# Kernel optimization log

Hardware: AMD Instinct MI355X
Metric: run time of the kernel (lower is better)

The kernel has to match this reference:

```python
import jax, jax.numpy as jnp
import numpy as np

K = 255
L = 1.0 / K
W = L / 2.5
MU = (L * (jnp.arange(K, dtype=jnp.float32) + 0.5))  # [K]


def soft_hist(x):
    # x: [B, H, W] -> [B, K] soft histogram (mean of sigmoid-window memberships)
    B = x.shape[0]
    N = x.shape[1] * x.shape[2]
    xf = x.reshape(B, 1, -1)                      # [B, 1, N]
    d = xf - MU[None, :, None]                    # [B, K, N]
    pj = jax.nn.sigmoid((d + L / 2) / W) - jax.nn.sigmoid((d - L / 2) / W)
    return pj.sum(axis=2) / N                     # [B, K]


def emd(x, y):
    # matmul with lower-triangular ones == cumulative sum along bins
    cdf_x = jnp.cumsum(x, axis=1)
    cdf_y = jnp.cumsum(y, axis=1)
    return jnp.sum(jnp.square(cdf_x - cdf_y), axis=1)  # [B]


def setup_inputs() -> dict:
    key = jax.random.key(0)
    k1, k2 = jax.random.split(key)
    img = jax.random.uniform(k1, (8, 3, 256, 256), dtype=jnp.float32)
    img_t = jax.random.uniform(k2, (8, 3, 256, 256), dtype=jnp.float32)
    return {"img": img, "img_t": img_t}


def reference(img, img_t):
    r, g, b = img[:, 0], img[:, 1], img[:, 2]
    r_t, g_t, b_t = img_t[:, 0], img_t[:, 1], img_t[:, 2]
    r_hist = soft_hist(r)
    g_hist = soft_hist(g)
    b_hist = soft_hist(b)
    r_t_hist = soft_hist(r_t)  # computed but unused, faithful to original (bug: earth(r_hist, r_hist))
    g_t_hist = soft_hist(g_t)
    b_t_hist = soft_hist(b_t)
    loss = emd(r_hist, r_hist) + emd(g_hist, g_t_hist) + emd(b_hist, b_t_hist)
    return loss  # [B]
```

## Files before the change

### kernel.cpp

```cpp
#include <hip/hip_runtime.h>


#define NT 256
#define QF 32
#define FB 8160
#define FBP 8192
#define PAD 96
#define CNT_LDS 8448

__device__ __forceinline__ float fsigmoid(float z) {
    return __builtin_amdgcn_rcpf(1.0f + __expf(-z));
}

__global__ __launch_bounds__(NT) void fine_hist_kernel(
    const float* __restrict__ img, const float* __restrict__ img_t,
    unsigned* __restrict__ ws, int sub, int pix)
{
    const int blk = blockIdx.x;
    const int h   = blk / sub;
    const int s   = blk - h * sub;
    const int b   = h >> 2;
    const int ch  = 1 + ((h >> 1) & 1);
    const float* src = (h & 1) ? img_t : img;
    const float4* base = (const float4*)(src + (size_t)(b * 3 + ch) * 65536u
                                             + (size_t)s * (size_t)pix);

    __shared__ unsigned hist[FBP];
    #pragma unroll
    for (int r = 0; r < 8; ++r)
        ((uint4*)hist)[threadIdx.x + NT * r] = make_uint4(0u, 0u, 0u, 0u);
    __syncthreads();

    const int nv = pix >> 2;
    for (int i = threadIdx.x; i < nv; i += NT) {
        const float4 v = base[i];
        int j0 = (int)(v.x * 8160.0f);
        int j1 = (int)(v.y * 8160.0f);
        int j2 = (int)(v.z * 8160.0f);
        int j3 = (int)(v.w * 8160.0f);
        j0 = j0 < 0 ? 0 : (j0 > FB - 1 ? FB - 1 : j0);
        j1 = j1 < 0 ? 0 : (j1 > FB - 1 ? FB - 1 : j1);
        j2 = j2 < 0 ? 0 : (j2 > FB - 1 ? FB - 1 : j2);
        j3 = j3 < 0 ? 0 : (j3 > FB - 1 ? FB - 1 : j3);
        atomicAdd(&hist[j0], 1u);
        atomicAdd(&hist[j1], 1u);
        atomicAdd(&hist[j2], 1u);
        atomicAdd(&hist[j3], 1u);
    }
    __syncthreads();

    uint4* o = (uint4*)(ws + (size_t)blk * (size_t)FBP);
    #pragma unroll
    for (int r = 0; r < 8; ++r)
        o[threadIdx.x + NT * r] = ((uint4*)hist)[threadIdx.x + NT * r];
}

__global__ __launch_bounds__(NT) void cdf_kernel(
    const unsigned* __restrict__ ws, float* __restrict__ cdfout, int sub)
{
    const int h = blockIdx.x;
    const int k = threadIdx.x;

    __shared__ float cnt[CNT_LDS];
    __shared__ float coarse[NT];
    __shared__ float red[4];

    float4 acc[8];
    #pragma unroll
    for (int r = 0; r < 8; ++r) acc[r] = make_float4(0.f, 0.f, 0.f, 0.f);
    for (int s = 0; s < sub; ++s) {
        const uint4* p = (const uint4*)(ws + (size_t)(h * sub + s) * (size_t)FBP);
        #pragma unroll
        for (int r = 0; r < 8; ++r) {
            const uint4 u = p[k + NT * r];
            acc[r].x += (float)u.x; acc[r].y += (float)u.y;
            acc[r].z += (float)u.z; acc[r].w += (float)u.w;
        }
    }
    #pragma unroll
    for (int r = 0; r < 8; ++r)
        ((float4*)(cnt + PAD))[k + NT * r] = acc[r];
    if (k < PAD) cnt[k] = 0.0f;
    if (k < CNT_LDS - PAD - FBP) cnt[PAD + FBP + k] = 0.0f;
    __syncthreads();

    float cc = 0.0f;
    #pragma unroll
    for (int q = 0; q < QF; ++q) {
        const int qq = (q + k) & (QF - 1);
        cc += cnt[PAD + QF * k + qq];
    }
    coarse[k] = cc;
    __syncthreads();

    for (int off = 1; off < NT; off <<= 1) {
        const float v = (k + off < NT) ? coarse[k + off] : 0.0f;
        __syncthreads();
        coarse[k] += v;
        __syncthreads();
    }

    float s0t = cnt[PAD + k] * fsigmoid(2.5f * ((float)k + 0.5f) / 32.0f);
    #pragma unroll
    for (int off = 32; off; off >>= 1) s0t += __shfl_down(s0t, off);
    if ((k & 63) == 0) red[k >> 6] = s0t;
    __syncthreads();
    const float S0 = red[0] + red[1] + red[2] + red[3] + coarse[8];

    float t = 0.0f;
    const int jbase = PAD + QF * (k - 3);
    for (int i = 0; i < 256; ++i) {
        const int m = (i + k) & 255;
        const float sg = fsigmoid(2.5f * ((float)m + 0.5f) * (1.0f / 32.0f) - 10.0f);
        t += cnt[jbase + m] * sg;
    }
    const float ones = (k + 5 < NT) ? coarse[k + 5] : 0.0f;

    float cdf = 0.0f;
    if (k <= 254) cdf = (S0 - (t + ones)) * (1.0f / 65536.0f);
    cdfout[h * NT + k] = cdf;
}

__global__ __launch_bounds__(NT) void emd_kernel(
    const float* __restrict__ cdf, float* __restrict__ out)
{
    const int b = blockIdx.x;
    const int k = threadIdx.x;
    const float* c0 = cdf + (size_t)(b * 4 + 0) * NT;
    const float* c1 = cdf + (size_t)(b * 4 + 1) * NT;
    const float* c2 = cdf + (size_t)(b * 4 + 2) * NT;
    const float* c3 = cdf + (size_t)(b * 4 + 3) * NT;

    float v = 0.0f;
    if (k <= 254) {
        const float dg = c0[k] - c1[k];
        const float db = c2[k] - c3[k];
        v = dg * dg + db * db;
    }
    #pragma unroll
    for (int off = 32; off; off >>= 1) v += __shfl_down(v, off);
    __shared__ float red[4];
    if ((k & 63) == 0) red[k >> 6] = v;
    __syncthreads();
    if (k == 0) out[b] = red[0] + red[1] + red[2] + red[3];
}

extern "C" void kernel_launch(void* const* d_in, const int* in_sizes, int n_in,
                              void* d_out, int out_size, void* d_ws, size_t ws_size,
                              hipStream_t stream)
{
    const float* img   = (const float*)d_in[0];
    const float* img_t = (const float*)d_in[1];
    float* out = (float*)d_out;

    int SUB = 8;
    while (SUB > 1 &&
           (size_t)(32 * SUB) * FBP * 4u + 32u * NT * 4u > ws_size) SUB >>= 1;
    const int pix = 65536 / SUB;

    unsigned* ws_hist = (unsigned*)d_ws;
    float*    ws_cdf  = (float*)d_ws + (size_t)(32 * SUB) * FBP;

    hipLaunchKernelGGL(fine_hist_kernel, dim3(32 * SUB), dim3(NT), 0, stream,
                       img, img_t, ws_hist, SUB, pix);
    hipLaunchKernelGGL(cdf_kernel, dim3(32), dim3(NT), 0, stream,
                       ws_hist, ws_cdf, SUB);
    hipLaunchKernelGGL(emd_kernel, dim3(8), dim3(NT), 0, stream,
                       ws_cdf, out);
}
```

Before: 82.06 us.

## Halve fine-bin resolution, add parallel merge kernel, fuse CDF with EMD

The fine histogram drops from 8160 to 4080 bins (16 per coarse bin), which halves the LDS footprint and the partial-histogram traffic. Sub-splitting rises to 16 blocks per histogram. A new 256-block merge kernel sums the partials in parallel, replacing the 32-block serial accumulation inside the CDF kernel. CDF and EMD are fused into one 1024-thread block per batch item that uses a precomputed sigmoid table. The coarser fine bins approximate the sigmoid convolution less closely, which may affect accuracy.

```diff
diff --git a/kernel.cpp b/kernel.cpp
--- a/kernel.cpp
+++ b/kernel.cpp
@@ -1,47 +1,49 @@
 #include <hip/hip_runtime.h>
 
 
-#define NT 256
-#define QF 32
-#define FB 8160
-#define FBP 8192
-#define PAD 96
-#define CNT_LDS 8448
+#define QF 16
+#define FBINS 4096
+#define FBV 4080
+#define PADL 64
+#define CNTSZ (PADL + FBINS + 64)
 
 __device__ __forceinline__ float fsigmoid(float z) {
     return __builtin_amdgcn_rcpf(1.0f + __expf(-z));
 }
 
-__global__ __launch_bounds__(NT) void fine_hist_kernel(
+template<int SUB>
+__global__ __launch_bounds__(256) void fine_hist_kernel(
     const float* __restrict__ img, const float* __restrict__ img_t,
-    unsigned* __restrict__ ws, int sub, int pix)
+    unsigned* __restrict__ part)
 {
     const int blk = blockIdx.x;
-    const int h   = blk / sub;
-    const int s   = blk - h * sub;
+    const int h   = blk / SUB;
+    const int s   = blk - h * SUB;
     const int b   = h >> 2;
     const int ch  = 1 + ((h >> 1) & 1);
     const float* src = (h & 1) ? img_t : img;
+    const int pix = 65536 / SUB;
     const float4* base = (const float4*)(src + (size_t)(b * 3 + ch) * 65536u
                                              + (size_t)s * (size_t)pix);
 
-    __shared__ unsigned hist[FBP];
+    __shared__ unsigned hist[FBINS];
+    uint4* h4 = (uint4*)hist;
     #pragma unroll
-    for (int r = 0; r < 8; ++r)
-        ((uint4*)hist)[threadIdx.x + NT * r] = make_uint4(0u, 0u, 0u, 0u);
+    for (int r = 0; r < 4; ++r)
+        h4[threadIdx.x + 256 * r] = make_uint4(0u, 0u, 0u, 0u);
     __syncthreads();
 
     const int nv = pix >> 2;
-    for (int i = threadIdx.x; i < nv; i += NT) {
+    for (int i = threadIdx.x; i < nv; i += 256) {
         const float4 v = base[i];
-        int j0 = (int)(v.x * 8160.0f);
-        int j1 = (int)(v.y * 8160.0f);
-        int j2 = (int)(v.z * 8160.0f);
-        int j3 = (int)(v.w * 8160.0f);
-        j0 = j0 < 0 ? 0 : (j0 > FB - 1 ? FB - 1 : j0);
-        j1 = j1 < 0 ? 0 : (j1 > FB - 1 ? FB - 1 : j1);
-        j2 = j2 < 0 ? 0 : (j2 > FB - 1 ? FB - 1 : j2);
-        j3 = j3 < 0 ? 0 : (j3 > FB - 1 ? FB - 1 : j3);
+        int j0 = (int)(v.x * 4080.0f);
+        int j1 = (int)(v.y * 4080.0f);
+        int j2 = (int)(v.z * 4080.0f);
+        int j3 = (int)(v.w * 4080.0f);
+        j0 = j0 < 0 ? 0 : (j0 > FBV - 1 ? FBV - 1 : j0);
+        j1 = j1 < 0 ? 0 : (j1 > FBV - 1 ? FBV - 1 : j1);
+        j2 = j2 < 0 ? 0 : (j2 > FBV - 1 ? FBV - 1 : j2);
+        j3 = j3 < 0 ? 0 : (j3 > FBV - 1 ? FBV - 1 : j3);
         atomicAdd(&hist[j0], 1u);
         atomicAdd(&hist[j1], 1u);
         atomicAdd(&hist[j2], 1u);
@@ -49,100 +51,119 @@
     }
     __syncthreads();
 
-    uint4* o = (uint4*)(ws + (size_t)blk * (size_t)FBP);
+    uint4* o = (uint4*)(part + (size_t)blk * (size_t)FBINS);
     #pragma unroll
-    for (int r = 0; r < 8; ++r)
-        o[threadIdx.x + NT * r] = ((uint4*)hist)[threadIdx.x + NT * r];
+    for (int r = 0; r < 4; ++r)
+        o[threadIdx.x + 256 * r] = h4[threadIdx.x + 256 * r];
 }
 
-__global__ __launch_bounds__(NT) void cdf_kernel(
-    const unsigned* __restrict__ ws, float* __restrict__ cdfout, int sub)
+template<int SUB>
+__global__ __launch_bounds__(256) void merge_kernel(
+    const unsigned* __restrict__ part, unsigned* __restrict__ merged)
 {
-    const int h = blockIdx.x;
-    const int k = threadIdx.x;
+    const int h = blockIdx.x >> 3;
+    const int c = blockIdx.x & 7;
+    const int t = threadIdx.x;
+    const unsigned* p0 = part + (size_t)h * SUB * FBINS + c * 512 + 2 * t;
+    unsigned ax = 0u, ay = 0u;
+    #pragma unroll
+    for (int s = 0; s < SUB; ++s) {
+        const uint2 u = *(const uint2*)(p0 + (size_t)s * FBINS);
+        ax += u.x; ay += u.y;
+    }
+    *(uint2*)(merged + (size_t)h * FBINS + c * 512 + 2 * t) = make_uint2(ax, ay);
+}
 
-    __shared__ float cnt[CNT_LDS];
-    __shared__ float coarse[NT];
-    __shared__ float red[4];
+__global__ __launch_bounds__(1024) void cdf_emd_kernel(
+    const unsigned* __restrict__ merged, float* __restrict__ out)
+{
+    const int b   = blockIdx.x;
+    const int tid = threadIdx.x;
+    const int sg  = tid >> 8;
+    const int k   = tid & 255;
 
-    float4 acc[8];
+    __shared__ float cnt[4][CNTSZ];
+    __shared__ float coarse[4][256];
+    __shared__ float sgt[128];
+    __shared__ float s0red[16];
+    __shared__ float cdfs[4][256];
+    __shared__ float lred[16];
+
+    if (tid < 128)
+        sgt[tid] = fsigmoid((2.5f / 16.0f) * ((float)tid + 0.5f) - 10.0f);
+
+    const uint4* src = (const uint4*)(merged + (size_t)(b * 4 + sg) * FBINS);
+    float* cn = cnt[sg];
     #pragma unroll
-    for (int r = 0; r < 8; ++r) acc[r] = make_float4(0.f, 0.f, 0.f, 0.f);
-    for (int s = 0; s < sub; ++s) {
-        const uint4* p = (const uint4*)(ws + (size_t)(h * sub + s) * (size_t)FBP);
-        #pragma unroll
-        for (int r = 0; r < 8; ++r) {
-            const uint4 u = p[k + NT * r];
-            acc[r].x += (float)u.x; acc[r].y += (float)u.y;
-            acc[r].z += (float)u.z; acc[r].w += (float)u.w;
-        }
+    for (int r = 0; r < 4; ++r) {
+        const uint4 u = src[k + 256 * r];
+        *(float4*)(cn + PADL + 4 * (k + 256 * r)) =
+            make_float4((float)u.x, (float)u.y, (float)u.z, (float)u.w);
     }
-    #pragma unroll
-    for (int r = 0; r < 8; ++r)
-        ((float4*)(cnt + PAD))[k + NT * r] = acc[r];
-    if (k < PAD) cnt[k] = 0.0f;
-    if (k < CNT_LDS - PAD - FBP) cnt[PAD + FBP + k] = 0.0f;
+    if (k < PADL) cn[k] = 0.0f;
+    if (k < CNTSZ - PADL - FBINS) cn[PADL + FBINS + k] = 0.0f;
     __syncthreads();
 
     float cc = 0.0f;
     #pragma unroll
     for (int q = 0; q < QF; ++q) {
         const int qq = (q + k) & (QF - 1);
-        cc += cnt[PAD + QF * k + qq];
+        cc += cn[PADL + QF * k + qq];
     }
-    coarse[k] = cc;
+    coarse[sg][k] = cc;
+
+    float s0p = 0.0f;
+    if (k < 64) s0p = cn[PADL + k] * fsigmoid((2.5f / 16.0f) * ((float)k + 0.5f));
+    #pragma unroll
+    for (int off = 32; off; off >>= 1) s0p += __shfl_down(s0p, off);
+    if ((tid & 63) == 0) s0red[tid >> 6] = s0p;
+    __syncthreads();
+    const float S0w = s0red[4 * sg] + s0red[4 * sg + 1]
+                    + s0red[4 * sg + 2] + s0red[4 * sg + 3];
+
+    for (int off = 1; off < 256; off <<= 1) {
+        const float v = (k + off < 256) ? coarse[sg][k + off] : 0.0f;
+        __syncthreads();
+        coarse[sg][k] += v;
+        __syncthreads();
+    }
+    const float S0 = S0w + coarse[sg][4];
+
+    float t = 0.0f;
+    const int jb = PADL + QF * k - 48;
+    for (int i = 0; i < 128; ++i) {
+        const int m = (i + k) & 127;
+        t += cn[jb + m] * sgt[m];
+    }
+    const float ones = (k + 5 < 256) ? coarse[sg][k + 5] : 0.0f;
+
+    cdfs[sg][k] = (k <= 254) ? (S0 - t - ones) * (1.0f / 65536.0f) : 0.0f;
     __syncthreads();
 
-    for (int off = 1; off < NT; off <<= 1) {
-        const float v = (k + off < NT) ? coarse[k + off] : 0.0f;
-        __syncthreads();
-        coarse[k] += v;
-        __syncthreads();
+    if (tid < 256) {
+        const float dg = cdfs[0][tid] - cdfs[1][tid];
+        const float db = cdfs[2][tid] - cdfs[3][tid];
+        float v = dg * dg + db * db;
+        #pragma unroll
+        for (int off = 32; off; off >>= 1) v += __shfl_down(v, off);
+        if ((tid & 63) == 0) lred[tid >> 6] = v;
     }
-
-    float s0t = cnt[PAD + k] * fsigmoid(2.5f * ((float)k + 0.5f) / 32.0f);
-    #pragma unroll
-    for (int off = 32; off; off >>= 1) s0t += __shfl_down(s0t, off);
-    if ((k & 63) == 0) red[k >> 6] = s0t;
     __syncthreads();
-    const float S0 = red[0] + red[1] + red[2] + red[3] + coarse[8];
-
-    float t = 0.0f;
-    const int jbase = PAD + QF * (k - 3);
-    for (int i = 0; i < 256; ++i) {
-        const int m = (i + k) & 255;
-        const float sg = fsigmoid(2.5f * ((float)m + 0.5f) * (1.0f / 32.0f) - 10.0f);
-        t += cnt[jbase + m] * sg;
-    }
-    const float ones = (k + 5 < NT) ? coarse[k + 5] : 0.0f;
-
-    float cdf = 0.0f;
-    if (k <= 254) cdf = (S0 - (t + ones)) * (1.0f / 65536.0f);
-    cdfout[h * NT + k] = cdf;
+    if (tid == 0) out[b] = lred[0] + lred[1] + lred[2] + lred[3];
 }
 
-__global__ __launch_bounds__(NT) void emd_kernel(
-    const float* __restrict__ cdf, float* __restrict__ out)
+template<int SUB>
+static void launch_all(const float* img, const float* img_t, float* out,
+                       void* d_ws, hipStream_t stream)
 {
-    const int b = blockIdx.x;
-    const int k = threadIdx.x;
-    const float* c0 = cdf + (size_t)(b * 4 + 0) * NT;
-    const float* c1 = cdf + (size_t)(b * 4 + 1) * NT;
-    const float* c2 = cdf + (size_t)(b * 4 + 2) * NT;
-    const float* c3 = cdf + (size_t)(b * 4 + 3) * NT;
-
-    float v = 0.0f;
-    if (k <= 254) {
-        const float dg = c0[k] - c1[k];
-        const float db = c2[k] - c3[k];
-        v = dg * dg + db * db;
-    }
-    #pragma unroll
-    for (int off = 32; off; off >>= 1) v += __shfl_down(v, off);
-    __shared__ float red[4];
-    if ((k & 63) == 0) red[k >> 6] = v;
-    __syncthreads();
-    if (k == 0) out[b] = red[0] + red[1] + red[2] + red[3];
+    unsigned* part   = (unsigned*)d_ws;
+    unsigned* merged = part + (size_t)32 * SUB * FBINS;
+    hipLaunchKernelGGL(fine_hist_kernel<SUB>, dim3(32 * SUB), dim3(256), 0, stream,
+                       img, img_t, part);
+    hipLaunchKernelGGL(merge_kernel<SUB>, dim3(256), dim3(256), 0, stream,
+                       part, merged);
+    hipLaunchKernelGGL(cdf_emd_kernel, dim3(8), dim3(1024), 0, stream,
+                       merged, out);
 }
 
 extern "C" void kernel_launch(void* const* d_in, const int* in_sizes, int n_in,
@@ -153,18 +174,10 @@
     const float* img_t = (const float*)d_in[1];
     float* out = (float*)d_out;
 
-    int SUB = 8;
-    while (SUB > 1 &&
-           (size_t)(32 * SUB) * FBP * 4u + 32u * NT * 4u > ws_size) SUB >>= 1;
-    const int pix = 65536 / SUB;
+    const size_t need16 = ((size_t)32 * 16 + 32) * FBINS * 4u;
+    const size_t need4  = ((size_t)32 * 4  + 32) * FBINS * 4u;
 
-    unsigned* ws_hist = (unsigned*)d_ws;
-    float*    ws_cdf  = (float*)d_ws + (size_t)(32 * SUB) * FBP;
-
-    hipLaunchKernelGGL(fine_hist_kernel, dim3(32 * SUB), dim3(NT), 0, stream,
-                       img, img_t, ws_hist, SUB, pix);
-    hipLaunchKernelGGL(cdf_kernel, dim3(32), dim3(NT), 0, stream,
-                       ws_hist, ws_cdf, SUB);
-    hipLaunchKernelGGL(emd_kernel, dim3(8), dim3(NT), 0, stream,
-                       ws_cdf, out);
+    if (ws_size >= need16)      launch_all<16>(img, img_t, out, d_ws, stream);
+    else if (ws_size >= need4)  launch_all<4>(img, img_t, out, d_ws, stream);
+    else                        launch_all<1>(img, img_t, out, d_ws, stream);
 }
```

Measured after the change: 74.57 us. -9.1%, faster.
